# Performance work log

Hardware: AMD Instinct MI355X
Metric: run time of the kernel (lower is better)

The kernel has to match this reference:

```python
import jax, jax.numpy as jnp
import numpy as np

B, J, C, K, TOK, CH = 4096, 17, 512, 3, 256, 2048
EPS = 1e-5


def layernorm(x, g, b):
    m = jnp.mean(x, axis=-1, keepdims=True)
    v = jnp.mean(jnp.square(x - m), axis=-1, keepdims=True)
    return (x - m) / jnp.sqrt(v + EPS) * g + b


def gcn(x_bcj, W, b, adj):
    # 1x1 conv to K*C channels: (b,c,v) x (k,o,c) -> (b,k,o,v), then adjacency mix over v
    y = jnp.einsum('bcv,koc->bkov', x_bcj, W) + b[None, :, :, None]
    return jnp.einsum('bkov,kvw->bow', y, adj)  # (b, C, J)


def mlp(x, W1, b1, W2, b2):
    # torch Linear: y = x @ W.T + b ; GELU is exact (erf) in torch default
    h = jax.nn.gelu(x @ W1.T + b1, approximate=False)
    return h @ W2.T + b2


def setup_inputs() -> dict:
    key = jax.random.key(0)
    ks = jax.random.split(key, 8)
    s = lambda fan: 1.0 / np.sqrt(fan)
    return {
        'x': jax.random.normal(ks[0], (B, J, C), jnp.float32),
        'adj': jax.random.uniform(ks[1], (K, J, J), jnp.float32),
        'g1': jnp.ones((J,), jnp.float32), 'be1': jnp.zeros((J,), jnp.float32),
        'g2': jnp.ones((C,), jnp.float32), 'be2': jnp.zeros((C,), jnp.float32),
        'Wg1': jax.random.normal(ks[2], (K, C, C), jnp.float32) * s(C),
        'bg1': jnp.zeros((K, C), jnp.float32),
        'Wg2': jax.random.normal(ks[3], (K, C, C), jnp.float32) * s(C),
        'bg2': jnp.zeros((K, C), jnp.float32),
        'W11': jax.random.normal(ks[4], (TOK, J), jnp.float32) * s(J),
        'b11': jnp.zeros((TOK,), jnp.float32),
        'W12': jax.random.normal(ks[5], (J, TOK), jnp.float32) * s(TOK),
        'b12': jnp.zeros((J,), jnp.float32),
        'W21': jax.random.normal(ks[6], (CH, C), jnp.float32) * s(C),
        'b21': jnp.zeros((CH,), jnp.float32),
        'W22': jax.random.normal(ks[7], (C, CH), jnp.float32) * s(CH),
        'b22': jnp.zeros((C,), jnp.float32),
    }


def reference(x, adj, g1, be1, g2, be2, Wg1, bg1, Wg2, bg2,
              W11, b11, W12, b12, W21, b21, W22, b22):
    # model_type == 'graph_mlp'
    xt = jnp.transpose(x, (0, 2, 1))          # (B, C, J)
    res = xt
    xn = layernorm(xt, g1, be1)               # LN over J (length)
    g1_out = gcn(xn, Wg1, bg1, adj)           # (B, C, J)
    xt = res + mlp(xn, W11, b11, W12, b12) + g1_out
    x2 = jnp.transpose(xt, (0, 2, 1))         # (B, J, C)
    res = x2
    xn = layernorm(x2, g2, be2)               # LN over C (dim)
    g2_out = gcn(jnp.transpose(xn, (0, 2, 1)), Wg2, bg2, adj)  # (B, C, J)
    out = res + mlp(xn, W21, b21, W22, b22) + jnp.transpose(g2_out, (0, 2, 1))
    return out
```

## Files before the change

### kernel.cpp

```cpp
#include <hip/hip_runtime.h>
#include <hip/hip_bf16.h>

#define Bn   4096
#define Jn   17
#define Cn   512
#define Kn   3
#define TOKn 256
#define CHn  2048
#define EPSf 1e-5f
#define Mrows (Bn * Jn)

typedef unsigned short u16;
typedef short bf8_t __attribute__((ext_vector_type(8)));
typedef float f32x4 __attribute__((ext_vector_type(4)));

__device__ __forceinline__ float gelu_fast(float x) {
    float x2 = x * x;
    float z = x * __builtin_fmaf(0.1029474f, x2, 2.3022652f);
    float e = __builtin_amdgcn_exp2f(z);
    float r = __builtin_amdgcn_rcpf(e + 1.0f);
    return x * (1.0f - r);
}
__device__ __forceinline__ float bf2f(u16 u) {
    union { float f; unsigned int i; } w; w.i = ((unsigned int)u) << 16; return w.f;
}
__device__ __forceinline__ u16 f2bf(float f) {
    __hip_bfloat16 h = __float2bfloat16(f);
    union { __hip_bfloat16 h1; u16 u; } cv; cv.h1 = h; return cv.u;
}
__device__ __forceinline__ unsigned pk2(float a, float b) {
    float2 t; t.x = a; t.y = b;
    __hip_bfloat162 h = __float22bfloat162_rn(t);
    union { __hip_bfloat162 h2; unsigned u; } cv; cv.h2 = h; return cv.u;
}
__device__ __forceinline__ void unpack2(unsigned u, float& a, float& b) {
    union { float f; unsigned int i; } t;
    t.i = u << 16;          a = t.f;
    t.i = u & 0xffff0000u;  b = t.f;
}
__device__ __forceinline__ void gload_lds16(const void* g, void* l) {
    __builtin_amdgcn_global_load_lds(
        (const __attribute__((address_space(1))) void*)g,
        (__attribute__((address_space(3))) void*)l, 16, 0, 0);
}

__global__ __launch_bounds__(256) void prep_kernel(
    const float* __restrict__ W21, const float* __restrict__ W22,
    const float* __restrict__ Wg1, const float* __restrict__ Wg2,
    const float* __restrict__ bg1, const float* __restrict__ bg2,
    const float* __restrict__ adj,
    const float* __restrict__ W11, const float* __restrict__ W12,
    u16* __restrict__ W21b, u16* __restrict__ W22b,
    u16* __restrict__ Wg1t, u16* __restrict__ Wg2t,
    float* __restrict__ bias2a, float* __restrict__ bias2b,
    u16* __restrict__ W11p, u16* __restrict__ W12p)
{
    int bid = blockIdx.x, tid = threadIdx.x;
    if (bid < 1024) {
        const float* src = (bid < 512) ? W21 : W22;
        u16* dst = (bid < 512) ? W21b : W22b;
        size_t base = (size_t)(bid & 511) * 2048 + (size_t)tid * 8;
        float4 v0 = *(const float4*)(src + base);
        float4 v1 = *(const float4*)(src + base + 4);
        uint4 o;
        o.x = pk2(v0.x, v0.y); o.y = pk2(v0.z, v0.w);
        o.z = pk2(v1.x, v1.y); o.w = pk2(v1.z, v1.w);
        *(uint4*)(dst + base) = o;
    } else if (bid < 2048) {
        const float* src = (bid < 1536) ? Wg1 : Wg2;
        u16* dst = (bid < 1536) ? Wg1t : Wg2t;
        int rbase = ((bid - 1024) & 511) * 3;
        int c = tid * 2;
        for (int rr = 0; rr < 3; ++rr) {
            int ro = rbase + rr;
            int k = ro >> 9, o = ro & 511;
            const float* sp = src + ((size_t)k * Cn + o) * Cn + c;
            float2 v = *(const float2*)sp;
            *(unsigned*)(dst + (size_t)o * (Kn * Cn) + k * Cn + c) = pk2(v.x, v.y);
        }
    } else if (bid == 2048) {
        __shared__ float adjcs[Kn][Jn];
        for (int i = tid; i < Kn * Jn; i += 256) {
            int k = i / Jn, w = i - k * Jn;
            float s = 0.f;
            for (int v = 0; v < Jn; ++v) s += adj[k * (Jn * Jn) + v * Jn + w];
            adjcs[k][w] = s;
        }
        __syncthreads();
        for (int i = tid; i < Jn * Cn; i += 256) {
            int w = i >> 9, o = i & 511;
            float sa = 0.f, sb = 0.f;
            #pragma unroll
            for (int k = 0; k < Kn; ++k) {
                sa += bg1[k * Cn + o] * adjcs[k][w];
                sb += bg2[k * Cn + o] * adjcs[k][w];
            }
            bias2a[i] = sa; bias2b[i] = sb;
        }
    } else {
        for (int i = tid; i < 4 * TOKn * 8; i += 256) {
            int ck = i >> 11, t = (i >> 3) & 255, e = i & 7;
            int k = ck * 8 + e;
            W11p[i] = (k < Jn) ? f2bf(W11[t * Jn + k]) : (u16)0;
        }
        for (int idx = tid; idx < 32 * TOKn; idx += 256) {
            int j = idx >> 8, t = idx & 255;
            W12p[idx] = (j < Jn) ? f2bf(W12[j * TOKn + t]) : (u16)0;
        }
    }
}

template<int STAGE>
__global__ __launch_bounds__(256) void premix_kernel(
    const float* __restrict__ x,
    const u16* __restrict__ xn2,
    const float* __restrict__ adj,
    const float* __restrict__ g1, const float* __restrict__ be1,
    float* __restrict__ mean1, float* __restrict__ rstd1,
    u16* __restrict__ xmix)
{
    __shared__ float xsh[Jn][Cn];
    __shared__ float coef[Kn][Jn][Jn];
    __shared__ float s0sh[Kn][Jn];
    __shared__ float s1sh[Kn][Jn];
    __shared__ float msh[Cn], rsh[Cn];
    int b = blockIdx.x, tid = threadIdx.x;

    for (int i = tid; i < Kn * Jn * Jn; i += 256) {
        int k = i / (Jn * Jn); int rem = i - k * (Jn * Jn);
        int v = rem / Jn; int w = rem - v * Jn;
        float av = adj[i];
        coef[k][w][v] = (STAGE == 1) ? av * g1[v] : av;
    }
    if (STAGE == 1) {
        const float* xp = x + (size_t)b * (Jn * Cn);
        for (int i = tid; i < (Jn * Cn) / 4; i += 256)
            ((float4*)&xsh[0][0])[i] = ((const float4*)xp)[i];
    } else {
        const u16* xp = xn2 + (size_t)b * (Jn * Cn);
        for (int i = tid; i < (Jn * Cn) / 8; i += 256) {
            uint4 u = ((const uint4*)xp)[i];
            float* d = &(&xsh[0][0])[i * 8];
            unpack2(u.x, d[0], d[1]); unpack2(u.y, d[2], d[3]);
            unpack2(u.z, d[4], d[5]); unpack2(u.w, d[6], d[7]);
        }
    }
    __syncthreads();
    if (STAGE == 1) {
        for (int c = tid; c < Cn; c += 256) {
            float s = 0.f, q = 0.f;
            #pragma unroll
            for (int v = 0; v < Jn; ++v) { float t = xsh[v][c]; s += t; q += t * t; }
            float m = s * (1.0f / Jn);
            float var = fmaxf(q * (1.0f / Jn) - m * m, 0.f);
            float r = rsqrtf(var + EPSf);
            msh[c] = m; rsh[c] = r;
            mean1[(size_t)b * Cn + c] = m;
            rstd1[(size_t)b * Cn + c] = r;
        }
    }
    if (tid < Kn * Jn) {
        int k = tid / Jn, w = tid - k * Jn;
        float s0 = 0.f, s1 = 0.f;
        #pragma unroll
        for (int v = 0; v < Jn; ++v) {
            if (STAGE == 1) s0 += adj[k * (Jn * Jn) + v * Jn + w] * be1[v];
            s1 += coef[k][w][v];
        }
        s0sh[k][w] = s0; s1sh[k][w] = s1;
    }
    __syncthreads();
    u16* orow = xmix + (size_t)b * Jn * (Kn * Cn);
    int c = tid * 2;
    float m0v = 0.f, m1v = 0.f, r0v = 1.f, r1v = 1.f;
    if (STAGE == 1) { m0v = msh[c]; m1v = msh[c + 1]; r0v = rsh[c]; r1v = rsh[c + 1]; }
    for (int k = 0; k < Kn; ++k)
        for (int w = 0; w < Jn; ++w) {
            float cf[Jn];
            #pragma unroll
            for (int v = 0; v < Jn; ++v) cf[v] = coef[k][w][v];
            float d0 = 0.f, d1 = 0.f;
            #pragma unroll
            for (int v = 0; v < Jn; ++v) { d0 += cf[v] * xsh[v][c]; d1 += cf[v] * xsh[v][c + 1]; }
            float v0, v1;
            if (STAGE == 1) {
                float ss1 = s1sh[k][w], ss0 = s0sh[k][w];
                v0 = r0v * (d0 - m0v * ss1) + ss0;
                v1 = r1v * (d1 - m1v * ss1) + ss0;
            } else { v0 = d0; v1 = d1; }
            *(unsigned*)(orow + (size_t)w * (Kn * Cn) + k * Cn + c) = pk2(v0, v1);
        }
}

__global__ __launch_bounds__(256) void mlp1_mfma(
    const float* __restrict__ x,
    const float* __restrict__ mean1, const float* __restrict__ rstd1,
    const float* __restrict__ g1, const float* __restrict__ be1,
    const u16* __restrict__ W11p,
    const float* __restrict__ b11,
    const u16* __restrict__ W12p,
    const float* __restrict__ b12,
    float* __restrict__ out)
{
    __shared__ __align__(16) u16 As[128 * 40];
    __shared__ __align__(16) u16 Hs[128 * 128];
    __shared__ __align__(16) u16 W11s[4 * TOKn * 8];
    __shared__ __align__(16) u16 W12s[32 * TOKn];
    __shared__ __align__(16) float b11s[TOKn];
    __shared__ __align__(16) float msrs[256];
    __shared__ float g1s[32], be1s[32];

    int tid = threadIdx.x;
    int lane = tid & 63, wave = tid >> 6;
    int b = blockIdx.y, c0 = blockIdx.x * 128;
    const float* xb = x + (size_t)b * (Jn * Cn);

    #pragma unroll
    for (int t = 0; t < 4; ++t) {
        int idx = t * 256 + tid;
        gload_lds16(W11p + idx * 8, (char*)W11s + idx * 16);
    }
    #pragma unroll
    for (int t = 0; t < 4; ++t) {
        int idx = t * 256 + tid;
        int j = idx >> 5, s = idx & 31;
        gload_lds16(W12p + j * TOKn + ((s ^ (j & 7)) << 3), (char*)W12s + idx * 16);
    }
    if (wave == 0) gload_lds16(b11 + lane * 4, (char*)b11s + lane * 16);
    if (wave == 1) {
        const float* src = (lane < 32) ? (mean1 + (size_t)b * Cn + c0 + lane * 4)
                                       : (rstd1 + (size_t)b * Cn + c0 + (lane - 32) * 4);
        gload_lds16(src, (char*)msrs + lane * 16);
    }
    if (tid < Jn) { g1s[tid] = g1[tid]; be1s[tid] = be1[tid]; }
    asm volatile("s_waitcnt vmcnt(0)" ::: "memory");
    __syncthreads();

    const float* ms = msrs;
    const float* rs = msrs + 128;
    #pragma unroll
    for (int it = 0; it < 8; ++it) {
        int idx = it * 256 + tid;
        int r = idx & 127, k = (idx >> 7) << 1;
        float mr = ms[r], rr = rs[r];
        float v0 = 0.f, v1 = 0.f;
        if (k < Jn)     v0 = (xb[(size_t)k * Cn + c0 + r] - mr) * rr * g1s[k] + be1s[k];
        if (k + 1 < Jn) v1 = (xb[(size_t)(k + 1) * Cn + c0 + r] - mr) * rr * g1s[k + 1] + be1s[k + 1];
        int ck = (k >> 3) ^ ((r >> 3) & 3);
        *(unsigned*)((char*)As + r * 80 + (ck << 4) + ((k & 7) << 1)) = pk2(v0, v1);
    }
    __syncthreads();

    int rb = wave * 32;
    f32x4 acc2[2][2];
    #pragma unroll
    for (int i = 0; i < 2; ++i)
        #pragma unroll
        for (int j = 0; j < 2; ++j) acc2[i][j] = (f32x4)0.f;

    bf8_t bfc[2];
    #pragma unroll
    for (int cf = 0; cf < 2; ++cf) {
        int c = rb + cf * 16 + (lane & 15);
        int ck = (lane >> 4) ^ ((c >> 3) & 3);
        bfc[cf] = *(const bf8_t*)((const char*)As + c * 80 + (ck << 4));
    }

    #pragma unroll
    for (int ch = 0; ch < 2; ++ch) {
        f32x4 acc1[8][2];
        #pragma unroll
        for (int tf = 0; tf < 8; ++tf)
            #pragma unroll
            for (int cf = 0; cf < 2; ++cf) acc1[tf][cf] = (f32x4)0.f;
        #pragma unroll
        for (int tf = 0; tf < 8; ++tf) {
            int t = ch * 128 + tf * 16 + (lane & 15);
            bf8_t aw = *(const bf8_t*)((const char*)W11s + ((lane >> 4) << 12) + t * 16);
            #pragma unroll
            for (int cf = 0; cf < 2; ++cf)
                acc1[tf][cf] = __builtin_amdgcn_mfma_f32_16x16x32_bf16(aw, bfc[cf], acc1[tf][cf], 0, 0, 0);
        }
        #pragma unroll
        for (int tf = 0; tf < 8; ++tf) {
            int t0 = tf * 16 + ((lane >> 4) << 2);
            float bq0 = b11s[ch * 128 + t0 + 0];
            float bq1 = b11s[ch * 128 + t0 + 1];
            float bq2 = b11s[ch * 128 + t0 + 2];
            float bq3 = b11s[ch * 128 + t0 + 3];
            #pragma unroll
            for (int cf = 0; cf < 2; ++cf) {
                int c = rb + cf * 16 + (lane & 15);
                float h0 = gelu_fast(acc1[tf][cf][0] + bq0);
                float h1 = gelu_fast(acc1[tf][cf][1] + bq1);
                float h2 = gelu_fast(acc1[tf][cf][2] + bq2);
                float h3 = gelu_fast(acc1[tf][cf][3] + bq3);
                uint2 w; w.x = pk2(h0, h1); w.y = pk2(h2, h3);
                *(uint2*)((char*)Hs + c * 256 + ((((t0 >> 3) ^ (c & 7))) << 4) + ((t0 & 7) << 1)) = w;
            }
        }
        #pragma unroll
        for (int kt = 0; kt < 4; ++kt) {
            bf8_t bh[2];
            #pragma unroll
            for (int cf = 0; cf < 2; ++cf) {
                int c = rb + cf * 16 + (lane & 15);
                int tc = kt * 4 + (lane >> 4);
                bh[cf] = *(const bf8_t*)((const char*)Hs + c * 256 + ((tc ^ (c & 7)) << 4));
            }
            #pragma unroll
            for (int jf = 0; jf < 2; ++jf) {
                int j = jf * 16 + (lane & 15);
                int tc = ch * 16 + kt * 4 + (lane >> 4);
                bf8_t aw = *(const bf8_t*)((const char*)W12s + j * 512 + ((tc ^ (j & 7)) << 4));
                #pragma unroll
                for (int cf = 0; cf < 2; ++cf)
                    acc2[jf][cf] = __builtin_amdgcn_mfma_f32_16x16x32_bf16(aw, bh[cf], acc2[jf][cf], 0, 0, 0);
            }
        }
    }

    #pragma unroll
    for (int jf = 0; jf < 2; ++jf) {
        #pragma unroll
        for (int cf = 0; cf < 2; ++cf) {
            int c = c0 + rb + cf * 16 + (lane & 15);
            #pragma unroll
            for (int i = 0; i < 4; ++i) {
                int j = jf * 16 + ((lane >> 4) << 2) + i;
                if (j < Jn) {
                    size_t off = (size_t)b * (Jn * Cn) + (size_t)j * Cn + c;
                    out[off] = x[off] + acc2[jf][cf][i] + b12[j];
                }
            }
        }
    }
}

__global__ __launch_bounds__(256) void ln2_kernel(const float* __restrict__ X2,
        const float* __restrict__ g2, const float* __restrict__ be2,
        u16* __restrict__ xn2)
{
    int row = blockIdx.x * 4 + (threadIdx.x >> 6);
    int lane = threadIdx.x & 63;
    const float* p = X2 + (size_t)row * Cn;
    float4 v0 = ((const float4*)p)[lane];
    float4 v1 = ((const float4*)p)[lane + 64];
    float s = v0.x + v0.y + v0.z + v0.w + v1.x + v1.y + v1.z + v1.w;
    float q = v0.x*v0.x + v0.y*v0.y + v0.z*v0.z + v0.w*v0.w
            + v1.x*v1.x + v1.y*v1.y + v1.z*v1.z + v1.w*v1.w;
    #pragma unroll
    for (int off = 32; off > 0; off >>= 1) { s += __shfl_xor(s, off); q += __shfl_xor(q, off); }
    float mean = s * (1.0f / Cn);
    float var = fmaxf(q * (1.0f / Cn) - mean * mean, 0.f);
    float rs = rsqrtf(var + EPSf);
    float4 ga = ((const float4*)g2)[lane],      ba = ((const float4*)be2)[lane];
    float4 gb = ((const float4*)g2)[lane + 64], bb = ((const float4*)be2)[lane + 64];
    uint2 w0, w1;
    w0.x = pk2((v0.x-mean)*rs*ga.x + ba.x, (v0.y-mean)*rs*ga.y + ba.y);
    w0.y = pk2((v0.z-mean)*rs*ga.z + ba.z, (v0.w-mean)*rs*ga.w + ba.w);
    w1.x = pk2((v1.x-mean)*rs*gb.x + bb.x, (v1.y-mean)*rs*gb.y + bb.y);
    w1.y = pk2((v1.z-mean)*rs*gb.z + bb.z, (v1.w-mean)*rs*gb.w + bb.w);
    ((uint2*)(xn2 + (size_t)row * Cn))[lane] = w0;
    ((uint2*)(xn2 + (size_t)row * Cn))[lane + 64] = w1;
}

template<int EPI>
__global__ __launch_bounds__(256) void gemm_bt(
    const u16* __restrict__ A, int ldA,
    const u16* __restrict__ Bt, int ldB,
    int K, int Nld,
    const float* __restrict__ bias,
    float* __restrict__ outF, u16* __restrict__ outH)
{
    __shared__ __align__(16) u16 As[2][128 * 32];
    __shared__ __align__(16) u16 Bs[2][128 * 32];
    int tid = threadIdx.x;
    int gx = gridDim.x;
    int total = gx * gridDim.y;
    int lid = blockIdx.y * gx + blockIdx.x;
    int cpx = total >> 3;
    int wg = (lid & 7) * cpx + (lid >> 3);
    int n0 = (wg % gx) << 7;
    int m0 = (wg / gx) << 7;

    int wave = tid >> 6, lane = tid & 63;
    int wr = wave >> 1, wc = wave & 1;

    const u16* aSrc[2]; const u16* bSrc[2];
    #pragma unroll
    for (int t = 0; t < 2; ++t) {
        int idx = t * 256 + tid;
        int r = idx >> 2;
        int cs = (idx & 3) ^ ((r >> 1) & 3);
        aSrc[t] = A  + (size_t)(m0 + r) * ldA + cs * 8;
        bSrc[t] = Bt + (size_t)(n0 + r) * ldB + cs * 8;
    }
    int aOff[4], bOff[4];
    #pragma unroll
    for (int i = 0; i < 4; ++i) {
        int ra = wr * 64 + i * 16 + (lane & 15);
        aOff[i] = ra * 64 + ((((lane >> 4)) ^ ((ra >> 1) & 3)) << 4);
        int rb = wc * 64 + i * 16 + (lane & 15);
        bOff[i] = rb * 64 + ((((lane >> 4)) ^ ((rb >> 1) & 3)) << 4);
    }

    f32x4 acc[4][4];
    #pragma unroll
    for (int i = 0; i < 4; ++i)
        #pragma unroll
        for (int j = 0; j < 4; ++j) acc[i][j] = (f32x4)0.f;

    int KT = K >> 5;
    #pragma unroll
    for (int t = 0; t < 2; ++t) {
        int idx = t * 256 + tid;
        gload_lds16(aSrc[t], (char*)&As[0][0] + idx * 16);
        gload_lds16(bSrc[t], (char*)&Bs[0][0] + idx * 16);
    }
    int cur = 0;
    for (int kt = 0; kt < KT; ++kt) {
        asm volatile("s_waitcnt vmcnt(0)" ::: "memory");
        __syncthreads();
        if (kt + 1 < KT) {
            int k0 = (kt + 1) << 5;
            #pragma unroll
            for (int t = 0; t < 2; ++t) {
                int idx = t * 256 + tid;
                gload_lds16(aSrc[t] + k0, (char*)&As[cur ^ 1][0] + idx * 16);
                gload_lds16(bSrc[t] + k0, (char*)&Bs[cur ^ 1][0] + idx * 16);
            }
        }
        bf8_t af[4], bfr[4];
        #pragma unroll
        for (int i = 0; i < 4; ++i) {
            af[i]  = *(const bf8_t*)((const char*)&As[cur][0] + aOff[i]);
            bfr[i] = *(const bf8_t*)((const char*)&Bs[cur][0] + bOff[i]);
        }
        #pragma unroll
        for (int mi = 0; mi < 4; ++mi)
            #pragma unroll
            for (int ni = 0; ni < 4; ++ni)
                acc[mi][ni] = __builtin_amdgcn_mfma_f32_16x16x32_bf16(af[mi], bfr[ni], acc[mi][ni], 0, 0, 0);
        cur ^= 1;
    }

    #pragma unroll
    for (int mi = 0; mi < 4; ++mi) {
        int rbase = m0 + wr * 64 + mi * 16 + ((lane >> 4) << 2);
        #pragma unroll
        for (int ni = 0; ni < 4; ++ni) {
            int col = n0 + wc * 64 + ni * 16 + (lane & 15);
            if (EPI == 0) {
                float bv = bias[col];
                #pragma unroll
                for (int i = 0; i < 4; ++i) {
                    float v = gelu_fast(acc[mi][ni][i] + bv);
                    outH[(size_t)(rbase + i) * Nld + col] = f2bf(v);
                }
            } else if (EPI == 1) {
                float bv = bias ? bias[col] : 0.f;
                #pragma unroll
                for (int i = 0; i < 4; ++i) {
                    size_t off = (size_t)(rbase + i) * Nld + col;
                    outF[off] += acc[mi][ni][i] + bv;
                }
            } else {
                #pragma unroll
                for (int i = 0; i < 4; ++i) {
                    int row = rbase + i;
                    int w = row % Jn;
                    size_t off = (size_t)row * Nld + col;
                    outF[off] += acc[mi][ni][i] + bias[w * Cn + col];
                }
            }
        }
    }
}

extern "C" void kernel_launch(void* const* d_in, const int* in_sizes, int n_in,
                              void* d_out, int out_size, void* d_ws, size_t ws_size,
                              hipStream_t stream)
{
    (void)in_sizes; (void)n_in; (void)out_size;
    const float* x   = (const float*)d_in[0];
    const float* adj = (const float*)d_in[1];
    const float* g1  = (const float*)d_in[2];
    const float* be1 = (const float*)d_in[3];
    const float* g2  = (const float*)d_in[4];
    const float* be2 = (const float*)d_in[5];
    const float* Wg1 = (const float*)d_in[6];
    const float* bg1 = (const float*)d_in[7];
    const float* Wg2 = (const float*)d_in[8];
    const float* bg2 = (const float*)d_in[9];
    const float* W11 = (const float*)d_in[10];
    const float* b11 = (const float*)d_in[11];
    const float* W12 = (const float*)d_in[12];
    const float* b12 = (const float*)d_in[13];
    const float* W21 = (const float*)d_in[14];
    const float* b21 = (const float*)d_in[15];
    const float* W22 = (const float*)d_in[16];
    const float* b22 = (const float*)d_in[17];
    float* out = (float*)d_out;

    char* p = (char*)d_ws;
    float* mean1  = (float*)p;                 p += (size_t)Bn * Cn * 4;
    float* rstd1  = (float*)p;                 p += (size_t)Bn * Cn * 4;
    u16*   xn2    = (u16*)p;                   p += (size_t)Mrows * Cn * 2;
    u16*   W21b   = (u16*)p;                   p += (size_t)CHn * Cn * 2;
    u16*   W22b   = (u16*)p;                   p += (size_t)CHn * Cn * 2;
    u16*   Wg1t   = (u16*)p;                   p += (size_t)Cn * Kn * Cn * 2;
    u16*   Wg2t   = (u16*)p;                   p += (size_t)Cn * Kn * Cn * 2;
    float* bias2a = (float*)p;                 p += (size_t)Jn * Cn * 4;
    float* bias2b = (float*)p;                 p += (size_t)Jn * Cn * 4;
    u16*   W11p   = (u16*)p;                   p += (size_t)4 * TOKn * 8 * 2;
    u16*   W12p   = (u16*)p;                   p += (size_t)32 * TOKn * 2;
    u16*   xmix   = (u16*)p;
    u16*   Hbuf   = xmix;

    size_t fixedBytes = (size_t)((char*)xmix - (char*)d_ws);
    bool fullH = ws_size >= fixedBytes + (size_t)Mrows * CHn * 2;

    prep_kernel<<<2050, 256, 0, stream>>>(W21, W22, Wg1, Wg2, bg1, bg2, adj, W11, W12,
                                          W21b, W22b, Wg1t, Wg2t, bias2a, bias2b, W11p, W12p);
    premix_kernel<1><<<Bn, 256, 0, stream>>>(x, (const u16*)nullptr, adj, g1, be1, mean1, rstd1, xmix);
    {
        dim3 g(Cn / 128, Bn);
        mlp1_mfma<<<g, 256, 0, stream>>>(x, mean1, rstd1, g1, be1, W11p, b11, W12p, b12, out);
    }
    {
        dim3 g(Cn / 128, Mrows / 128);
        gemm_bt<2><<<g, 256, 0, stream>>>(xmix, Kn * Cn, Wg1t, Kn * Cn, Kn * Cn, Cn, bias2a, out, (u16*)nullptr);
    }
    ln2_kernel<<<Mrows / 4, 256, 0, stream>>>(out, g2, be2, xn2);
    if (fullH) {
        dim3 ga(CHn / 128, Mrows / 128);
        gemm_bt<0><<<ga, 256, 0, stream>>>(xn2, Cn, W21b, Cn, Cn, CHn, b21, (float*)nullptr, Hbuf);
        dim3 gb(Cn / 128, Mrows / 128);
        gemm_bt<1><<<gb, 256, 0, stream>>>(Hbuf, CHn, W22b, CHn, CHn, Cn, b22, out, (u16*)nullptr);
    } else {
        for (int h = 0; h < 2; ++h) {
            int hc = h * 1024;
            dim3 ga(1024 / 128, Mrows / 128);
            gemm_bt<0><<<ga, 256, 0, stream>>>(xn2, Cn, W21b + (size_t)hc * Cn, Cn, Cn, 1024, b21 + hc, (float*)nullptr, Hbuf);
            dim3 gb(Cn / 128, Mrows / 128);
            gemm_bt<1><<<gb, 256, 0, stream>>>(Hbuf, 1024, W22b + hc, CHn, 1024, Cn, (h == 0) ? b22 : (const float*)nullptr, out, (u16*)nullptr);
        }
    }
    premix_kernel<2><<<Bn, 256, 0, stream>>>((const float*)nullptr, xn2, adj, (const float*)nullptr, (const float*)nullptr,
                                             (float*)nullptr, (float*)nullptr, xmix);
    {
        dim3 g(Cn / 128, Mrows / 128);
        gemm_bt<2><<<g, 256, 0, stream>>>(xmix, Kn * Cn, Wg2t, Kn * Cn, Kn * Cn, Cn, bias2b, out, (u16*)nullptr);
    }
}
```

Baseline: 1.631 ms.

## Enlarge GEMM tiles to 256x256 with 512 threads and 4-stage LDS pipeline

Reworks the bf16 MFMA GEMM to compute 256x256 output tiles with 8 waves, each holding an 8x4 grid of 16x16 accumulators. The single-stage double buffer becomes a 4-slot ring with three K-slices prefetched ahead, using counted vmcnt waits and raw barriers in place of a full drain every step. It also raises MFMA issue priority with setprio. The aim is more data reuse per tile and better hiding of global load latency. The cost is higher register use, 128KB of LDS, and fewer blocks (Mrows/256 = 272 rows of tiles, with only 2 column tiles for the N=512 GEMMs), which may underfill the GPU.

```diff
diff --git a/kernel.cpp b/kernel.cpp
--- a/kernel.cpp
+++ b/kernel.cpp
@@ -366,96 +366,117 @@
 }
 
 template<int EPI>
-__global__ __launch_bounds__(256) void gemm_bt(
+__global__ __launch_bounds__(512) void gemm_bt(
     const u16* __restrict__ A, int ldA,
     const u16* __restrict__ Bt, int ldB,
     int K, int Nld,
     const float* __restrict__ bias,
     float* __restrict__ outF, u16* __restrict__ outH)
 {
-    __shared__ __align__(16) u16 As[2][128 * 32];
-    __shared__ __align__(16) u16 Bs[2][128 * 32];
+    __shared__ __align__(16) u16 As[4 * 8192];
+    __shared__ __align__(16) u16 Bs[4 * 8192];
+
     int tid = threadIdx.x;
     int gx = gridDim.x;
     int total = gx * gridDim.y;
     int lid = blockIdx.y * gx + blockIdx.x;
     int cpx = total >> 3;
     int wg = (lid & 7) * cpx + (lid >> 3);
-    int n0 = (wg % gx) << 7;
-    int m0 = (wg / gx) << 7;
+    int n0 = (wg % gx) << 8;
+    int m0 = (wg / gx) << 8;
 
     int wave = tid >> 6, lane = tid & 63;
-    int wr = wave >> 1, wc = wave & 1;
-
-    const u16* aSrc[2]; const u16* bSrc[2];
-    #pragma unroll
-    for (int t = 0; t < 2; ++t) {
-        int idx = t * 256 + tid;
-        int r = idx >> 2;
-        int cs = (idx & 3) ^ ((r >> 1) & 3);
-        aSrc[t] = A  + (size_t)(m0 + r) * ldA + cs * 8;
-        bSrc[t] = Bt + (size_t)(n0 + r) * ldB + cs * 8;
-    }
-    int aOff[4], bOff[4];
-    #pragma unroll
-    for (int i = 0; i < 4; ++i) {
-        int ra = wr * 64 + i * 16 + (lane & 15);
-        aOff[i] = ra * 64 + ((((lane >> 4)) ^ ((ra >> 1) & 3)) << 4);
-        int rb = wc * 64 + i * 16 + (lane & 15);
-        bOff[i] = rb * 64 + ((((lane >> 4)) ^ ((rb >> 1) & 3)) << 4);
-    }
-
-    f32x4 acc[4][4];
-    #pragma unroll
-    for (int i = 0; i < 4; ++i)
-        #pragma unroll
-        for (int j = 0; j < 4; ++j) acc[i][j] = (f32x4)0.f;
-
-    int KT = K >> 5;
-    #pragma unroll
-    for (int t = 0; t < 2; ++t) {
-        int idx = t * 256 + tid;
-        gload_lds16(aSrc[t], (char*)&As[0][0] + idx * 16);
-        gload_lds16(bSrc[t], (char*)&Bs[0][0] + idx * 16);
-    }
-    int cur = 0;
-    for (int kt = 0; kt < KT; ++kt) {
-        asm volatile("s_waitcnt vmcnt(0)" ::: "memory");
-        __syncthreads();
-        if (kt + 1 < KT) {
-            int k0 = (kt + 1) << 5;
-            #pragma unroll
-            for (int t = 0; t < 2; ++t) {
-                int idx = t * 256 + tid;
-                gload_lds16(aSrc[t] + k0, (char*)&As[cur ^ 1][0] + idx * 16);
-                gload_lds16(bSrc[t] + k0, (char*)&Bs[cur ^ 1][0] + idx * 16);
-            }
-        }
-        bf8_t af[4], bfr[4];
-        #pragma unroll
-        for (int i = 0; i < 4; ++i) {
-            af[i]  = *(const bf8_t*)((const char*)&As[cur][0] + aOff[i]);
-            bfr[i] = *(const bf8_t*)((const char*)&Bs[cur][0] + bOff[i]);
-        }
-        #pragma unroll
-        for (int mi = 0; mi < 4; ++mi)
-            #pragma unroll
-            for (int ni = 0; ni < 4; ++ni)
-                acc[mi][ni] = __builtin_amdgcn_mfma_f32_16x16x32_bf16(af[mi], bfr[ni], acc[mi][ni], 0, 0, 0);
-        cur ^= 1;
-    }
-
-    #pragma unroll
-    for (int mi = 0; mi < 4; ++mi) {
-        int rbase = m0 + wr * 64 + mi * 16 + ((lane >> 4) << 2);
-        #pragma unroll
-        for (int ni = 0; ni < 4; ++ni) {
-            int col = n0 + wc * 64 + ni * 16 + (lane & 15);
+    int wr = wave >> 2, wc = wave & 3;
+    int q = lane >> 4, li = lane & 15;
+
+    int idxs[2] = { tid, 512 + tid };
+    const u16* aP[2]; const u16* bP[2];
+    char* aL[2]; char* bL[2];
+    #pragma unroll
+    for (int p = 0; p < 2; ++p) {
+        int r = idxs[p] >> 2, cq = idxs[p] & 3;
+        int sw = ((cq ^ (r & 3)) << 3);
+        aP[p] = A  + (size_t)(m0 + r) * ldA + sw;
+        bP[p] = Bt + (size_t)(n0 + r) * ldB + sw;
+        aL[p] = (char*)As + idxs[p] * 16;
+        bL[p] = (char*)Bs + idxs[p] * 16;
+    }
+
+    int aByte[8], bByte[4];
+    #pragma unroll
+    for (int m = 0; m < 8; ++m) {
+        int row = wr * 128 + m * 16 + li;
+        aByte[m] = row * 64 + ((q ^ (row & 3)) << 4);
+    }
+    #pragma unroll
+    for (int n = 0; n < 4; ++n) {
+        int row = wc * 64 + n * 16 + li;
+        bByte[n] = row * 64 + ((q ^ (row & 3)) << 4);
+    }
+
+    f32x4 acc[8][4];
+    #pragma unroll
+    for (int m = 0; m < 8; ++m)
+        #pragma unroll
+        for (int n = 0; n < 4; ++n) acc[m][n] = (f32x4)0.f;
+
+    int NS = K >> 5;
+    #pragma unroll
+    for (int sl = 0; sl < 3; ++sl) {
+        int slot = sl, k0 = sl << 5;
+        #pragma unroll
+        for (int p = 0; p < 2; ++p) {
+            gload_lds16(aP[p] + k0, aL[p] + slot * 16384);
+            gload_lds16(bP[p] + k0, bL[p] + slot * 16384);
+        }
+    }
+
+    for (int s = 0; s < NS; ++s) {
+        if (s + 3 < NS) {
+            int slot = (s + 3) & 3, k0 = (s + 3) << 5;
+            #pragma unroll
+            for (int p = 0; p < 2; ++p) {
+                gload_lds16(aP[p] + k0, aL[p] + slot * 16384);
+                gload_lds16(bP[p] + k0, bL[p] + slot * 16384);
+            }
+        }
+        int rem = NS - 1 - s;
+        if (rem >= 3)      asm volatile("s_waitcnt vmcnt(12)" ::: "memory");
+        else if (rem == 2) asm volatile("s_waitcnt vmcnt(8)" ::: "memory");
+        else if (rem == 1) asm volatile("s_waitcnt vmcnt(4)" ::: "memory");
+        else               asm volatile("s_waitcnt vmcnt(0)" ::: "memory");
+        asm volatile("s_barrier" ::: "memory");
+
+        const char* aBase = (const char*)As + (s & 3) * 16384;
+        const char* bBase = (const char*)Bs + (s & 3) * 16384;
+        bf8_t af[8], bfv[4];
+        #pragma unroll
+        for (int m = 0; m < 8; ++m) af[m] = *(const bf8_t*)(aBase + aByte[m]);
+        #pragma unroll
+        for (int n = 0; n < 4; ++n) bfv[n] = *(const bf8_t*)(bBase + bByte[n]);
+        __builtin_amdgcn_s_setprio(1);
+        #pragma unroll
+        for (int m = 0; m < 8; ++m)
+            #pragma unroll
+            for (int n = 0; n < 4; ++n)
+                acc[m][n] = __builtin_amdgcn_mfma_f32_16x16x32_bf16(af[m], bfv[n], acc[m][n], 0, 0, 0);
+        __builtin_amdgcn_s_setprio(0);
+        __builtin_amdgcn_sched_barrier(0);
+        asm volatile("s_waitcnt lgkmcnt(0)" ::: "memory");
+        asm volatile("s_barrier" ::: "memory");
+    }
+
+    #pragma unroll
+    for (int m = 0; m < 8; ++m) {
+        int rbase = m0 + wr * 128 + m * 16 + ((lane >> 4) << 2);
+        #pragma unroll
+        for (int n = 0; n < 4; ++n) {
+            int col = n0 + wc * 64 + n * 16 + li;
             if (EPI == 0) {
                 float bv = bias[col];
                 #pragma unroll
                 for (int i = 0; i < 4; ++i) {
-                    float v = gelu_fast(acc[mi][ni][i] + bv);
+                    float v = gelu_fast(acc[m][n][i] + bv);
                     outH[(size_t)(rbase + i) * Nld + col] = f2bf(v);
                 }
             } else if (EPI == 1) {
@@ -463,7 +484,7 @@
                 #pragma unroll
                 for (int i = 0; i < 4; ++i) {
                     size_t off = (size_t)(rbase + i) * Nld + col;
-                    outF[off] += acc[mi][ni][i] + bv;
+                    outF[off] += acc[m][n][i] + bv;
                 }
             } else {
                 #pragma unroll
@@ -471,7 +492,7 @@
                     int row = rbase + i;
                     int w = row % Jn;
                     size_t off = (size_t)row * Nld + col;
-                    outF[off] += acc[mi][ni][i] + bias[w * Cn + col];
+                    outF[off] += acc[m][n][i] + bias[w * Cn + col];
                 }
             }
         }
@@ -529,28 +550,28 @@
         mlp1_mfma<<<g, 256, 0, stream>>>(x, mean1, rstd1, g1, be1, W11p, b11, W12p, b12, out);
     }
     {
-        dim3 g(Cn / 128, Mrows / 128);
-        gemm_bt<2><<<g, 256, 0, stream>>>(xmix, Kn * Cn, Wg1t, Kn * Cn, Kn * Cn, Cn, bias2a, out, (u16*)nullptr);
+        dim3 g(Cn / 256, Mrows / 256);
+        gemm_bt<2><<<g, 512, 0, stream>>>(xmix, Kn * Cn, Wg1t, Kn * Cn, Kn * Cn, Cn, bias2a, out, (u16*)nullptr);
     }
     ln2_kernel<<<Mrows / 4, 256, 0, stream>>>(out, g2, be2, xn2);
     if (fullH) {
-        dim3 ga(CHn / 128, Mrows / 128);
-        gemm_bt<0><<<ga, 256, 0, stream>>>(xn2, Cn, W21b, Cn, Cn, CHn, b21, (float*)nullptr, Hbuf);
-        dim3 gb(Cn / 128, Mrows / 128);
-        gemm_bt<1><<<gb, 256, 0, stream>>>(Hbuf, CHn, W22b, CHn, CHn, Cn, b22, out, (u16*)nullptr);
+        dim3 ga(CHn / 256, Mrows / 256);
+        gemm_bt<0><<<ga, 512, 0, stream>>>(xn2, Cn, W21b, Cn, Cn, CHn, b21, (float*)nullptr, Hbuf);
+        dim3 gb(Cn / 256, Mrows / 256);
+        gemm_bt<1><<<gb, 512, 0, stream>>>(Hbuf, CHn, W22b, CHn, CHn, Cn, b22, out, (u16*)nullptr);
     } else {
         for (int h = 0; h < 2; ++h) {
             int hc = h * 1024;
-            dim3 ga(1024 / 128, Mrows / 128);
-            gemm_bt<0><<<ga, 256, 0, stream>>>(xn2, Cn, W21b + (size_t)hc * Cn, Cn, Cn, 1024, b21 + hc, (float*)nullptr, Hbuf);
-            dim3 gb(Cn / 128, Mrows / 128);
-            gemm_bt<1><<<gb, 256, 0, stream>>>(Hbuf, 1024, W22b + hc, CHn, 1024, Cn, (h == 0) ? b22 : (const float*)nullptr, out, (u16*)nullptr);
+            dim3 ga(1024 / 256, Mrows / 256);
+            gemm_bt<0><<<ga, 512, 0, stream>>>(xn2, Cn, W21b + (size_t)hc * Cn, Cn, Cn, 1024, b21 + hc, (float*)nullptr, Hbuf);
+            dim3 gb(Cn / 256, Mrows / 256);
+            gemm_bt<1><<<gb, 512, 0, stream>>>(Hbuf, 1024, W22b + hc, CHn, 1024, Cn, (h == 0) ? b22 : (const float*)nullptr, out, (u16*)nullptr);
         }
     }
     premix_kernel<2><<<Bn, 256, 0, stream>>>((const float*)nullptr, xn2, adj, (const float*)nullptr, (const float*)nullptr,
                                              (float*)nullptr, (float*)nullptr, xmix);
     {
-        dim3 g(Cn / 128, Mrows / 128);
-        gemm_bt<2><<<g, 256, 0, stream>>>(xmix, Kn * Cn, Wg2t, Kn * Cn, Kn * Cn, Cn, bias2b, out, (u16*)nullptr);
-    }
-}
+        dim3 g(Cn / 256, Mrows / 256);
+        gemm_bt<2><<<g, 512, 0, stream>>>(xmix, Kn * Cn, Wg2t, Kn * Cn, Kn * Cn, Cn, bias2b, out, (u16*)nullptr);
+    }
+}
```

New measurement: 2.029 ms. +24.4%, slower.

## Concatenate MLP2 down-projection and GCN2 GEMMs along K into one GEMM

Applied to the files above, without the earlier changes.

The second-stage MLP down-projection (H·W22ᵀ) and the second GCN GEMM (xmix·Wg2ᵀ) both accumulate into the same output. They are merged into a single GEMM over a concatenated K dimension of CHn+3·Cn. The GELU output and the premixed activations are written side by side into one wide buffer, and a combined bf16 weight matrix plus a merged bias are built in prep. This removes one read-modify-write pass over the fp32 output and one kernel launch, at the cost of a larger workspace requirement, with a fallback when the workspace is too small.

```diff
diff --git a/kernel.cpp b/kernel.cpp
--- a/kernel.cpp
+++ b/kernel.cpp
@@ -9,6 +9,7 @@
 #define CHn  2048
 #define EPSf 1e-5f
 #define Mrows (Bn * Jn)
+#define KCAT (CHn + Kn * Cn)
 
 typedef unsigned short u16;
 typedef short bf8_t __attribute__((ext_vector_type(8)));
@@ -50,10 +51,12 @@
     const float* __restrict__ bg1, const float* __restrict__ bg2,
     const float* __restrict__ adj,
     const float* __restrict__ W11, const float* __restrict__ W12,
+    const float* __restrict__ b22,
     u16* __restrict__ W21b, u16* __restrict__ W22b,
     u16* __restrict__ Wg1t, u16* __restrict__ Wg2t,
-    float* __restrict__ bias2a, float* __restrict__ bias2b,
-    u16* __restrict__ W11p, u16* __restrict__ W12p)
+    float* __restrict__ bias2a, float* __restrict__ bias2b, float* __restrict__ bias2bc,
+    u16* __restrict__ W11p, u16* __restrict__ W12p,
+    u16* __restrict__ Wcomb)
 {
     int bid = blockIdx.x, tid = threadIdx.x;
     if (bid < 1024) {
@@ -95,9 +98,9 @@
                 sa += bg1[k * Cn + o] * adjcs[k][w];
                 sb += bg2[k * Cn + o] * adjcs[k][w];
             }
-            bias2a[i] = sa; bias2b[i] = sb;
-        }
-    } else {
+            bias2a[i] = sa; bias2b[i] = sb; bias2bc[i] = sb + b22[o];
+        }
+    } else if (bid == 2049) {
         for (int i = tid; i < 4 * TOKn * 8; i += 256) {
             int ck = i >> 11, t = (i >> 3) & 255, e = i & 7;
             int k = ck * 8 + e;
@@ -106,6 +109,18 @@
         for (int idx = tid; idx < 32 * TOKn; idx += 256) {
             int j = idx >> 8, t = idx & 255;
             W12p[idx] = (j < Jn) ? f2bf(W12[j * TOKn + t]) : (u16)0;
+        }
+    } else {
+        int o = bid - 2050;
+        for (int idx = tid; idx < KCAT; idx += 256) {
+            float v;
+            if (idx < CHn) v = W22[(size_t)o * CHn + idx];
+            else {
+                int rem = idx - CHn;
+                int k = rem >> 9, c = rem & 511;
+                v = Wg2[((size_t)k * Cn + o) * Cn + c];
+            }
+            Wcomb[(size_t)o * KCAT + idx] = f2bf(v);
         }
     }
 }
@@ -117,7 +132,7 @@
     const float* __restrict__ adj,
     const float* __restrict__ g1, const float* __restrict__ be1,
     float* __restrict__ mean1, float* __restrict__ rstd1,
-    u16* __restrict__ xmix)
+    u16* __restrict__ xmix, int oStride, int oColOff)
 {
     __shared__ float xsh[Jn][Cn];
     __shared__ float coef[Kn][Jn][Jn];
@@ -170,7 +185,7 @@
         s0sh[k][w] = s0; s1sh[k][w] = s1;
     }
     __syncthreads();
-    u16* orow = xmix + (size_t)b * Jn * (Kn * Cn);
+    u16* orow = xmix + (size_t)b * Jn * oStride + oColOff;
     int c = tid * 2;
     float m0v = 0.f, m1v = 0.f, r0v = 1.f, r1v = 1.f;
     if (STAGE == 1) { m0v = msh[c]; m1v = msh[c + 1]; r0v = rsh[c]; r1v = rsh[c + 1]; }
@@ -188,7 +203,7 @@
                 v0 = r0v * (d0 - m0v * ss1) + ss0;
                 v1 = r1v * (d1 - m1v * ss1) + ss0;
             } else { v0 = d0; v1 = d1; }
-            *(unsigned*)(orow + (size_t)w * (Kn * Cn) + k * Cn + c) = pk2(v0, v1);
+            *(unsigned*)(orow + (size_t)w * oStride + k * Cn + c) = pk2(v0, v1);
         }
 }
 
@@ -369,7 +384,7 @@
 __global__ __launch_bounds__(256) void gemm_bt(
     const u16* __restrict__ A, int ldA,
     const u16* __restrict__ Bt, int ldB,
-    int K, int Nld,
+    int K, int ldOut,
     const float* __restrict__ bias,
     float* __restrict__ outF, u16* __restrict__ outH)
 {
@@ -456,13 +471,13 @@
                 #pragma unroll
                 for (int i = 0; i < 4; ++i) {
                     float v = gelu_fast(acc[mi][ni][i] + bv);
-                    outH[(size_t)(rbase + i) * Nld + col] = f2bf(v);
+                    outH[(size_t)(rbase + i) * ldOut + col] = f2bf(v);
                 }
             } else if (EPI == 1) {
                 float bv = bias ? bias[col] : 0.f;
                 #pragma unroll
                 for (int i = 0; i < 4; ++i) {
-                    size_t off = (size_t)(rbase + i) * Nld + col;
+                    size_t off = (size_t)(rbase + i) * ldOut + col;
                     outF[off] += acc[mi][ni][i] + bv;
                 }
             } else {
@@ -470,7 +485,7 @@
                 for (int i = 0; i < 4; ++i) {
                     int row = rbase + i;
                     int w = row % Jn;
-                    size_t off = (size_t)row * Nld + col;
+                    size_t off = (size_t)row * ldOut + col;
                     outF[off] += acc[mi][ni][i] + bias[w * Cn + col];
                 }
             }
@@ -511,19 +526,24 @@
     u16*   W22b   = (u16*)p;                   p += (size_t)CHn * Cn * 2;
     u16*   Wg1t   = (u16*)p;                   p += (size_t)Cn * Kn * Cn * 2;
     u16*   Wg2t   = (u16*)p;                   p += (size_t)Cn * Kn * Cn * 2;
+    u16*   Wcomb  = (u16*)p;                   p += (size_t)Cn * KCAT * 2;
     float* bias2a = (float*)p;                 p += (size_t)Jn * Cn * 4;
     float* bias2b = (float*)p;                 p += (size_t)Jn * Cn * 4;
+    float* bias2bc= (float*)p;                 p += (size_t)Jn * Cn * 4;
     u16*   W11p   = (u16*)p;                   p += (size_t)4 * TOKn * 8 * 2;
     u16*   W12p   = (u16*)p;                   p += (size_t)32 * TOKn * 2;
     u16*   xmix   = (u16*)p;
     u16*   Hbuf   = xmix;
 
     size_t fixedBytes = (size_t)((char*)xmix - (char*)d_ws);
-    bool fullH = ws_size >= fixedBytes + (size_t)Mrows * CHn * 2;
-
-    prep_kernel<<<2050, 256, 0, stream>>>(W21, W22, Wg1, Wg2, bg1, bg2, adj, W11, W12,
-                                          W21b, W22b, Wg1t, Wg2t, bias2a, bias2b, W11p, W12p);
-    premix_kernel<1><<<Bn, 256, 0, stream>>>(x, (const u16*)nullptr, adj, g1, be1, mean1, rstd1, xmix);
+    bool combined = ws_size >= fixedBytes + (size_t)Mrows * KCAT * 2;
+    bool fullH    = ws_size >= fixedBytes + (size_t)Mrows * CHn * 2;
+
+    prep_kernel<<<2562, 256, 0, stream>>>(W21, W22, Wg1, Wg2, bg1, bg2, adj, W11, W12, b22,
+                                          W21b, W22b, Wg1t, Wg2t, bias2a, bias2b, bias2bc,
+                                          W11p, W12p, Wcomb);
+    premix_kernel<1><<<Bn, 256, 0, stream>>>(x, (const u16*)nullptr, adj, g1, be1, mean1, rstd1,
+                                             xmix, Kn * Cn, 0);
     {
         dim3 g(Cn / 128, Bn);
         mlp1_mfma<<<g, 256, 0, stream>>>(x, mean1, rstd1, g1, be1, W11p, b11, W12p, b12, out);
@@ -533,24 +553,40 @@
         gemm_bt<2><<<g, 256, 0, stream>>>(xmix, Kn * Cn, Wg1t, Kn * Cn, Kn * Cn, Cn, bias2a, out, (u16*)nullptr);
     }
     ln2_kernel<<<Mrows / 4, 256, 0, stream>>>(out, g2, be2, xn2);
-    if (fullH) {
-        dim3 ga(CHn / 128, Mrows / 128);
-        gemm_bt<0><<<ga, 256, 0, stream>>>(xn2, Cn, W21b, Cn, Cn, CHn, b21, (float*)nullptr, Hbuf);
-        dim3 gb(Cn / 128, Mrows / 128);
-        gemm_bt<1><<<gb, 256, 0, stream>>>(Hbuf, CHn, W22b, CHn, CHn, Cn, b22, out, (u16*)nullptr);
+    if (combined) {
+        u16* HX = xmix;
+        {
+            dim3 ga(CHn / 128, Mrows / 128);
+            gemm_bt<0><<<ga, 256, 0, stream>>>(xn2, Cn, W21b, Cn, Cn, KCAT, b21, (float*)nullptr, HX);
+        }
+        premix_kernel<2><<<Bn, 256, 0, stream>>>((const float*)nullptr, xn2, adj, (const float*)nullptr,
+                                                 (const float*)nullptr, (float*)nullptr, (float*)nullptr,
+                                                 HX, KCAT, CHn);
+        {
+            dim3 g(Cn / 128, Mrows / 128);
+            gemm_bt<2><<<g, 256, 0, stream>>>(HX, KCAT, Wcomb, KCAT, KCAT, Cn, bias2bc, out, (u16*)nullptr);
+        }
     } else {
-        for (int h = 0; h < 2; ++h) {
-            int hc = h * 1024;
-            dim3 ga(1024 / 128, Mrows / 128);
-            gemm_bt<0><<<ga, 256, 0, stream>>>(xn2, Cn, W21b + (size_t)hc * Cn, Cn, Cn, 1024, b21 + hc, (float*)nullptr, Hbuf);
+        if (fullH) {
+            dim3 ga(CHn / 128, Mrows / 128);
+            gemm_bt<0><<<ga, 256, 0, stream>>>(xn2, Cn, W21b, Cn, Cn, CHn, b21, (float*)nullptr, Hbuf);
             dim3 gb(Cn / 128, Mrows / 128);
-            gemm_bt<1><<<gb, 256, 0, stream>>>(Hbuf, 1024, W22b + hc, CHn, 1024, Cn, (h == 0) ? b22 : (const float*)nullptr, out, (u16*)nullptr);
-        }
-    }
-    premix_kernel<2><<<Bn, 256, 0, stream>>>((const float*)nullptr, xn2, adj, (const float*)nullptr, (const float*)nullptr,
-                                             (float*)nullptr, (float*)nullptr, xmix);
-    {
-        dim3 g(Cn / 128, Mrows / 128);
-        gemm_bt<2><<<g, 256, 0, stream>>>(xmix, Kn * Cn, Wg2t, Kn * Cn, Kn * Cn, Cn, bias2b, out, (u16*)nullptr);
-    }
-}
+            gemm_bt<1><<<gb, 256, 0, stream>>>(Hbuf, CHn, W22b, CHn, CHn, Cn, b22, out, (u16*)nullptr);
+        } else {
+            for (int h = 0; h < 2; ++h) {
+                int hc = h * 1024;
+                dim3 ga(1024 / 128, Mrows / 128);
+                gemm_bt<0><<<ga, 256, 0, stream>>>(xn2, Cn, W21b + (size_t)hc * Cn, Cn, Cn, 1024, b21 + hc, (float*)nullptr, Hbuf);
+                dim3 gb(Cn / 128, Mrows / 128);
+                gemm_bt<1><<<gb, 256, 0, stream>>>(Hbuf, 1024, W22b + hc, CHn, 1024, Cn, (h == 0) ? b22 : (const float*)nullptr, out, (u16*)nullptr);
+            }
+        }
+        premix_kernel<2><<<Bn, 256, 0, stream>>>((const float*)nullptr, xn2, adj, (const float*)nullptr,
+                                                 (const float*)nullptr, (float*)nullptr, (float*)nullptr,
+                                                 xmix, Kn * Cn, 0);
+        {
+            dim3 g(Cn / 128, Mrows / 128);
+            gemm_bt<2><<<g, 256, 0, stream>>>(xmix, Kn * Cn, Wg2t, Kn * Cn, Kn * Cn, Cn, bias2b, out, (u16*)nullptr);
+        }
+    }
+}
```

Result: no change. 1.636 ms (+0.3%).
